# Optimization experiments

Measured on AMD Instinct MI355X. Metric: run time of the kernel, lower is better.

The kernel has to match this reference:

```python
import jax, jax.numpy as jnp
import numpy as np

B, L, T = 512, 1024, 128  # batch, seq_len, n_tags


def setup_inputs() -> dict:
    key = jax.random.key(0)
    k1, k2, k3 = jax.random.split(key, 3)
    return {
        "emit_scores": jax.random.normal(k1, (B, L, T), dtype=jnp.float32),
        "transitions": jax.random.normal(k2, (T, T), dtype=jnp.float32),
        "tag_weight": jax.random.uniform(k3, (T,), dtype=jnp.float32),
    }


def _viterbi_single(emit, transitions):
    # emit: [L, T] (already scaled by tag_weight); transitions: [T, T]
    def step(prev, obs):
        # scores[i, j] = prev[i] + obs[j] + transitions[i, j]
        scores = prev[:, None] + obs[None, :] + transitions  # [T, T]
        return jnp.max(scores, axis=0), jnp.argmax(scores, axis=0).astype(jnp.int32)

    prev, bps = jax.lax.scan(step, emit[0], emit[1:])  # bps: [L-1, T]
    best_score = jnp.max(prev)
    last = jnp.argmax(prev).astype(jnp.int32)

    # Backtrace: path[t] = bps[t][path[t+1]], path[L-1] = last
    def back(idx, bp):
        nidx = bp[idx]
        return nidx, nidx

    _, rev_path = jax.lax.scan(back, last, bps, reverse=True)  # [L-1]
    path = jnp.concatenate([rev_path, last[None]])  # [L]
    return path, best_score


def reference(emit_scores, transitions, tag_weight):
    # emit_scores *= tag_weight (broadcast over tag dim), matching the torch code
    emit = emit_scores * tag_weight  # [B, L, T]
    path, best_score = jax.vmap(_viterbi_single, in_axes=(0, None))(emit, transitions)
    # path: [B, L] int32 tag indices (the original maps these to tag strings);
    # best_score: [B] Viterbi max score.
    return path, best_score
```

## Files before the change

kernel.cpp:

```cpp
#include <hip/hip_runtime.h>

#define B 512
#define L 1024
#define T 128
#define NROWS (L - 1)
#define SEG 64
#define NSEG 16

typedef unsigned char u8;
typedef float f2 __attribute__((ext_vector_type(2)));

#if __has_builtin(__builtin_elementwise_max)
#define MAX2(a, b) __builtin_elementwise_max((a), (b))
#else
static __device__ __forceinline__ f2 max2_(f2 a, f2 b) {
    f2 r; r.x = fmaxf(a.x, b.x); r.y = fmaxf(a.y, b.y); return r;
}
#define MAX2(a, b) max2_((a), (b))
#endif
#define M3(a, b, c) fmaxf(fmaxf((a), (b)), (c))

#define BAR()                                                  \
    do {                                                       \
        asm volatile("s_waitcnt lgkmcnt(0)" ::: "memory");     \
        __builtin_amdgcn_s_barrier();                          \
        asm volatile("" ::: "memory");                         \
    } while (0)


__global__ __launch_bounds__(512, 4) void viterbi_fwd_val(
    const float* __restrict__ emit, const float* __restrict__ trans,
    const float* __restrict__ w, float* __restrict__ out,
    float* __restrict__ prevws, int* __restrict__ lastTag)
{
    const int b   = blockIdx.x;
    const int tid = threadIdx.x;
    const int h   = tid & 3;
    const int j   = tid >> 2;
    const int hbase = h << 5;
    const bool lane0 = (h == 0);

    __shared__ __align__(16) float prevbuf[2 * T];
    __shared__ float swv[8];
    __shared__ int   swj[8];

    f2 tc2[16];
#pragma unroll
    for (int q = 0; q < 8; ++q) {
        f2 a, c;
        a.x = trans[(size_t)(hbase + 4 * q + 0) * T + j];
        a.y = trans[(size_t)(hbase + 4 * q + 1) * T + j];
        c.x = trans[(size_t)(hbase + 4 * q + 2) * T + j];
        c.y = trans[(size_t)(hbase + 4 * q + 3) * T + j];
        tc2[2 * q] = a; tc2[2 * q + 1] = c;
    }

    const float wj = w[j];
    const size_t ebase = (size_t)b * L * T;
    float* prow = prevws + (size_t)b * NROWS * T;

    const char* prd = (const char*)prevbuf + 128 * h;
    char* pwr = (char*)prevbuf + 16 * ((j >> 2) ^ (j >> 5)) + 4 * (j & 3);

    const float e0 = emit[ebase + j] * wj;
    if (lane0) *(float*)pwr = e0;
    if (h == 1) prow[j] = e0;
    float myprev = e0;
    float r_c = emit[ebase + (size_t)T + j];
    float r_1 = emit[ebase + (size_t)2 * T + j];
    float bv_prev = 0.0f;
    BAR();

#define STEP(T_, ROFF_, WOFF_)                                                 \
    {                                                                          \
        const int t_ = (T_);                                                   \
        if (h == 1 && t_ >= 2)                                                 \
            prow[(size_t)(t_ - 1) * T + j] = bv_prev;                          \
        const int tn_ = (t_ + 2 < L) ? (t_ + 2) : (L - 1);                     \
        const float r_2 = emit[ebase + (size_t)tn_ * T + j];                   \
        const float obs_ = r_c * wj;                                           \
        f2 od_; od_.x = obs_; od_.y = obs_;                                    \
        f2 sv[16];                                                             \
        _Pragma("unroll")                                                      \
        for (int q = 0; q < 8; ++q) {                                          \
            const float4 p = *(const float4*)(prd + (ROFF_) + 16 * (q ^ h));   \
            f2 plo; plo.x = p.x; plo.y = p.y;                                  \
            f2 phi; phi.x = p.z; phi.y = p.w;                                  \
            sv[2 * q]     = (plo + od_) + tc2[2 * q];                          \
            sv[2 * q + 1] = (phi + od_) + tc2[2 * q + 1];                      \
        }                                                                      \
        const f2 a0 = MAX2(sv[0], sv[1]),   a1 = MAX2(sv[2], sv[3]);           \
        const f2 a2 = MAX2(sv[4], sv[5]),   a3 = MAX2(sv[6], sv[7]);           \
        const f2 a4 = MAX2(sv[8], sv[9]),   a5 = MAX2(sv[10], sv[11]);         \
        const f2 a6 = MAX2(sv[12], sv[13]), a7 = MAX2(sv[14], sv[15]);         \
        const f2 b0 = MAX2(a0, a1), b1 = MAX2(a2, a3);                         \
        const f2 b2 = MAX2(a4, a5), b3 = MAX2(a6, a7);                         \
        const f2 c0 = MAX2(b0, b1), c1 = MAX2(b2, b3);                         \
        const f2 d0 = MAX2(c0, c1);                                            \
        float bv = fmaxf(d0.x, d0.y);                                          \
        bv = fmaxf(bv, __shfl_xor(bv, 1));                                     \
        bv = fmaxf(bv, __shfl_xor(bv, 2));                                     \
        if (lane0) *(float*)(pwr + (WOFF_)) = bv;                              \
        myprev = bv;                                                           \
        bv_prev = bv;                                                          \
        r_c = r_1; r_1 = r_2;                                                  \
        BAR();                                                                 \
    }

    int t = 1;
    while (t + 1 < L) {
        STEP(t, 0, 512)
        STEP(t + 1, 512, 0)
        t += 2;
    }
    STEP(1023, 0, 512)
#undef STEP

    float rv = myprev; int rj = j;
#pragma unroll
    for (int m = 4; m <= 32; m <<= 1) {
        const float pv = __shfl_xor(rv, m);
        const int   pj = __shfl_xor(rj, m);
        if (pv > rv || (pv == rv && pj < rj)) { rv = pv; rj = pj; }
    }
    if ((tid & 63) == 0) { swv[tid >> 6] = rv; swj[tid >> 6] = rj; }
    __syncthreads();
    if (tid == 0) {
        float fv = swv[0]; int fj = swj[0];
#pragma unroll
        for (int wv = 1; wv < 8; ++wv) {
            if (swv[wv] > fv || (swv[wv] == fv && swj[wv] < fj)) {
                fv = swv[wv]; fj = swj[wv];
            }
        }
        out[(size_t)B * L + b] = fv;
        out[(size_t)b * L + (L - 1)] = (float)fj;
        lastTag[b] = fj;
    }
}

__global__ __launch_bounds__(64, 1) void backtrace(
    const float* __restrict__ emit, const float* __restrict__ trans,
    const float* __restrict__ w, const float* __restrict__ prevws,
    const int* __restrict__ lastTag, float* __restrict__ out)
{
    const int b = blockIdx.x;
    const int lane = threadIdx.x;
    __shared__ float transT[T * T];

#pragma unroll 4
    for (int it = 0; it < (T * T) / 64; ++it) {
        const int k = it * 64 + lane;
        const int i = k >> 7, jj = k & 127;
        transT[jj * T + (i ^ (jj & 31))] = trans[k];
    }

    const float w0 = w[lane], w1 = w[lane + 64];
    const size_t pbase = (size_t)b * NROWS * T;
    const size_t ebase = (size_t)b * L * T;
    const size_t obase = (size_t)b * L;

    float rp0[8], rp1[8], re0[8], re1[8];
#pragma unroll
    for (int k = 0; k < 8; ++k) {
        rp0[k] = prevws[pbase + (size_t)(1022 - k) * T + lane];
        rp1[k] = prevws[pbase + (size_t)(1022 - k) * T + lane + 64];
        re0[k] = emit[ebase + (size_t)(1023 - k) * T + lane];
        re1[k] = emit[ebase + (size_t)(1023 - k) * T + lane + 64];
    }

    int idx = lastTag[b];
    const float bsc = out[(size_t)B * L + b];
    float pp0 = bsc, pp1 = bsc;
    __syncthreads();

    int r = 1022;

#define BODY(U_)                                                               \
    {                                                                          \
        const float c0_ = rp0[U_], c1_ = rp1[U_];                              \
        const float e0_ = re0[U_], e1_ = re1[U_];                              \
        const int pr = (r >= 8) ? (r - 8) : 0;                                 \
        rp0[U_] = prevws[pbase + (size_t)pr * T + lane];                       \
        rp1[U_] = prevws[pbase + (size_t)pr * T + lane + 64];                  \
        re0[U_] = emit[ebase + (size_t)(pr + 1) * T + lane];                   \
        re1[U_] = emit[ebase + (size_t)(pr + 1) * T + lane + 64];              \
        const int sl = idx & 63;                                               \
        const bool lo = idx < 64;                                              \
        const float bv  = __shfl(lo ? pp0 : pp1, sl);                          \
        const float ew0 = e0_ * w0, ew1 = e1_ * w1;                            \
        const float obs = __shfl(lo ? ew0 : ew1, sl);                          \
        const int xc = lane ^ (idx & 31);                                      \
        const float t0 = transT[idx * T + xc];                                 \
        const float t1 = transT[idx * T + 64 + xc];                            \
        const float s0 = (c0_ + obs) + t0;                                     \
        const float s1 = (c1_ + obs) + t1;                                     \
        const unsigned long long m0 = __ballot(s0 == bv);                      \
        const unsigned long long m1 = __ballot(s1 == bv);                      \
        idx = (m0 != 0ULL) ? __builtin_ctzll(m0)                               \
                           : 64 + __builtin_ctzll(m1);                         \
        if (lane == 0) out[obase + r] = (float)idx;                            \
        pp0 = c0_; pp1 = c1_;                                                  \
        --r;                                                                   \
    }

#pragma unroll 1
    for (int g = 0; g < 127; ++g) {
        BODY(0) BODY(1) BODY(2) BODY(3) BODY(4) BODY(5) BODY(6) BODY(7)
    }
    BODY(0) BODY(1) BODY(2) BODY(3) BODY(4) BODY(5) BODY(6)
#undef BODY
}

__global__ __launch_bounds__(512, 4) void viterbi_fwd_slow(
    const float* __restrict__ emit, const float* __restrict__ trans,
    const float* __restrict__ w, float* __restrict__ out,
    u8* __restrict__ bps, int* __restrict__ lastTag)
{
    const int b   = blockIdx.x;
    const int tid = threadIdx.x;
    const int h   = tid & 3;
    const int j   = tid >> 2;
    const int hbase = h << 5;
    const bool lane0 = (h == 0);
    const int INF = 0x7fffffff;

    __shared__ __align__(16) float prevbuf[2 * T];
    __shared__ float swv[8];
    __shared__ int   swj[8];

    f2 tc2[16];
#pragma unroll
    for (int q = 0; q < 8; ++q) {
        f2 a, c;
        a.x = trans[(size_t)(hbase + 4 * q + 0) * T + j];
        a.y = trans[(size_t)(hbase + 4 * q + 1) * T + j];
        c.x = trans[(size_t)(hbase + 4 * q + 2) * T + j];
        c.y = trans[(size_t)(hbase + 4 * q + 3) * T + j];
        tc2[2 * q] = a; tc2[2 * q + 1] = c;
    }

    const float wj = w[j];
    const size_t ebase = (size_t)b * L * T;
    u8* bprow = bps + (size_t)b * NROWS * T;

    const char* prd = (const char*)prevbuf + 128 * h;
    char* pwr = (char*)prevbuf + 16 * ((j >> 2) ^ (j >> 5)) + 4 * (j & 3);

    const float e0 = emit[ebase + j] * wj;
    if (lane0) *(float*)pwr = e0;
    float myprev = e0;
    float raw_cur = emit[ebase + (size_t)T + j];
    int bidx_prev = 0;
    __syncthreads();

#define STEP(T_, ROFF_, WOFF_)                                                 \
    {                                                                          \
        const int t_ = (T_);                                                   \
        if (lane0 && t_ >= 2)                                                  \
            bprow[(size_t)(t_ - 2) * T + j] = (u8)bidx_prev;                   \
        const int tn_ = (t_ + 1 < L) ? (t_ + 1) : (L - 1);                     \
        const float raw_next_ = emit[ebase + (size_t)tn_ * T + j];             \
        const float obs_ = raw_cur * wj;                                       \
        f2 od_; od_.x = obs_; od_.y = obs_;                                    \
        f2 sv[16];                                                             \
        _Pragma("unroll")                                                      \
        for (int q = 0; q < 8; ++q) {                                          \
            const float4 p = *(const float4*)(prd + (ROFF_) + 16 * (q ^ h));   \
            f2 plo; plo.x = p.x; plo.y = p.y;                                  \
            f2 phi; phi.x = p.z; phi.y = p.w;                                  \
            sv[2 * q]     = (plo + od_) + tc2[2 * q];                          \
            sv[2 * q + 1] = (phi + od_) + tc2[2 * q + 1];                      \
        }                                                                      \
        float cm[4]; int loc[4];                                               \
        _Pragma("unroll")                                                      \
        for (int c = 0; c < 4; ++c) {                                          \
            const float s0 = sv[4 * c + 0].x, s1 = sv[4 * c + 0].y;            \
            const float s2 = sv[4 * c + 1].x, s3 = sv[4 * c + 1].y;            \
            const float s4 = sv[4 * c + 2].x, s5 = sv[4 * c + 2].y;            \
            const float s6 = sv[4 * c + 3].x, s7 = sv[4 * c + 3].y;            \
            const float m = M3(M3(s0, s1, s2), M3(s3, s4, s5),                 \
                               fmaxf(s6, s7));                                 \
            int k = 0;                                                         \
            k = (s7 == m) ? 7 : k; k = (s6 == m) ? 6 : k;                      \
            k = (s5 == m) ? 5 : k; k = (s4 == m) ? 4 : k;                      \
            k = (s3 == m) ? 3 : k; k = (s2 == m) ? 2 : k;                      \
            k = (s1 == m) ? 1 : k;                                             \
            cm[c] = m; loc[c] = 8 * c + k;                                     \
        }                                                                      \
        float bv = fmaxf(fmaxf(cm[0], cm[1]), fmaxf(cm[2], cm[3]));            \
        const int l0 = (cm[0] == bv) ? loc[0] : INF;                           \
        const int l1 = (cm[1] == bv) ? loc[1] : INF;                           \
        const int l2 = (cm[2] == bv) ? loc[2] : INF;                           \
        const int l3 = (cm[3] == bv) ? loc[3] : INF;                           \
        const int lm = min(min(min(l0, l1), l2), l3);                          \
        int gi = hbase + lm;                                                   \
        const float lv = bv;                                                   \
        bv = fmaxf(bv, __shfl_xor(bv, 1));                                     \
        bv = fmaxf(bv, __shfl_xor(bv, 2));                                     \
        int ii = (lv == bv) ? gi : INF;                                        \
        ii = min(ii, __shfl_xor(ii, 1));                                       \
        ii = min(ii, __shfl_xor(ii, 2));                                       \
        if (lane0) *(float*)(pwr + (WOFF_)) = bv;                              \
        myprev = bv;                                                           \
        bidx_prev = ii;                                                        \
        raw_cur = raw_next_;                                                   \
        __syncthreads();                                                       \
    }

    int t = 1;
    while (t + 1 < L) {
        STEP(t, 0, 512)
        STEP(t + 1, 512, 0)
        t += 2;
    }
    STEP(1023, 0, 512)
#undef STEP

    if (lane0) bprow[(size_t)(NROWS - 1) * T + j] = (u8)bidx_prev;

    float rv = myprev; int rj = j;
#pragma unroll
    for (int m = 4; m <= 32; m <<= 1) {
        const float pv = __shfl_xor(rv, m);
        const int   pj = __shfl_xor(rj, m);
        if (pv > rv || (pv == rv && pj < rj)) { rv = pv; rj = pj; }
    }
    if ((tid & 63) == 0) { swv[tid >> 6] = rv; swj[tid >> 6] = rj; }
    __syncthreads();
    if (tid == 0) {
        float fv = swv[0]; int fj = swj[0];
#pragma unroll
        for (int wv = 1; wv < 8; ++wv) {
            if (swv[wv] > fv || (swv[wv] == fv && swj[wv] < fj)) {
                fv = swv[wv]; fj = swj[wv];
            }
        }
        out[(size_t)B * L + b] = fv;
        out[(size_t)b * L + (L - 1)] = (float)fj;
        lastTag[b] = fj;
    }
}

__global__ __launch_bounds__(T) void segcomp(const u8* __restrict__ bps,
                                             u8* __restrict__ comp)
{
    const int s = blockIdx.x & (NSEG - 1);
    const int b = blockIdx.x >> 4;
    const int r0 = s * SEG;
    const int cnt = (NROWS - r0 < SEG) ? (NROWS - r0) : SEG;

    __shared__ __align__(16) u8 rows[SEG * T];
    const uint4* src = (const uint4*)(bps + ((size_t)b * NROWS + r0) * T);
    uint4* dst = (uint4*)rows;
    const int nvec = cnt * (T / 16);
    for (int k = threadIdx.x; k < nvec; k += T) dst[k] = src[k];
    __syncthreads();

    int x = threadIdx.x;
    for (int k = cnt - 1; k >= 0; --k) x = rows[k * T + x];
    comp[((size_t)b * NSEG + s) * T + threadIdx.x] = (u8)x;
}

__global__ void chainseg(const u8* __restrict__ comp,
                         const int* __restrict__ lastTag,
                         float* __restrict__ out)
{
    const int b = blockIdx.x * blockDim.x + threadIdx.x;
    if (b >= B) return;
    int e = lastTag[b];
#pragma unroll 1
    for (int s = NSEG - 1; s >= 0; --s) {
        e = comp[((size_t)b * NSEG + s) * T + e];
        out[(size_t)b * L + s * SEG] = (float)e;
    }
}

__global__ __launch_bounds__(T) void fillseg(const u8* __restrict__ bps,
                                             const int* __restrict__ lastTag,
                                             float* __restrict__ out)
{
    const int s = blockIdx.x & (NSEG - 1);
    const int b = blockIdx.x >> 4;
    const int r0 = s * SEG;
    const int cnt = (NROWS - r0 < SEG) ? (NROWS - r0) : SEG;

    __shared__ __align__(16) u8 rows[SEG * T];
    const uint4* src = (const uint4*)(bps + ((size_t)b * NROWS + r0) * T);
    uint4* dst = (uint4*)rows;
    const int nvec = cnt * (T / 16);
    for (int k = threadIdx.x; k < nvec; k += T) dst[k] = src[k];
    __syncthreads();

    if (threadIdx.x == 0) {
        int e = (s == NSEG - 1) ? lastTag[b]
                                : (int)out[(size_t)b * L + (size_t)(s + 1) * SEG];
        for (int k = cnt - 1; k >= 1; --k) {
            e = rows[k * T + e];
            out[(size_t)b * L + r0 + k] = (float)e;
        }
    }
}

extern "C" void kernel_launch(void* const* d_in, const int* in_sizes, int n_in,
                              void* d_out, int out_size, void* d_ws, size_t ws_size,
                              hipStream_t stream)
{
    const float* emit  = (const float*)d_in[0];
    const float* trans = (const float*)d_in[1];
    const float* w     = (const float*)d_in[2];
    float* out = (float*)d_out;

    const size_t prev_bytes = (size_t)B * NROWS * T * sizeof(float);
    const size_t need_fast  = prev_bytes + B * sizeof(int);

    if (ws_size >= need_fast) {
        float* prevws  = (float*)d_ws;
        int*   lastTag = (int*)((char*)d_ws + prev_bytes);
        viterbi_fwd_val<<<B, 512, 0, stream>>>(emit, trans, w, out, prevws, lastTag);
        backtrace<<<B, 64, 0, stream>>>(emit, trans, w, prevws, lastTag, out);
    } else {
        u8*  bps     = (u8*)d_ws;
        u8*  comp    = bps + (size_t)B * NROWS * T;
        int* lastTag = (int*)(comp + (size_t)B * NSEG * T);
        viterbi_fwd_slow<<<B, 512, 0, stream>>>(emit, trans, w, out, bps, lastTag);
        segcomp<<<B * NSEG, T, 0, stream>>>(bps, comp);
        chainseg<<<2, 256, 0, stream>>>(comp, lastTag, out);
        fillseg<<<B * NSEG, T, 0, stream>>>(bps, lastTag, out);
    }
}
```

Baseline: 877.7 us.

## Run forward Viterbi pass with one wavefront per sequence, dropping block barriers

The forward max-plus recursion now runs in a single 64-lane wavefront per batch element instead of a 512-thread block. Each lane owns two tags, keeps its full transition column in registers (256 floats), and uses packed adds and max3 inline asm. This removes per-step block barriers and the cross-lane shuffle reductions. In exchange each step does 32x more work per lane serially, register pressure is very high, and occupancy is limited to 512 waves total. The backtrace also gets a fallback when no lane matches.

```diff
diff --git a/kernel.cpp b/kernel.cpp
--- a/kernel.cpp
+++ b/kernel.cpp
@@ -10,15 +10,18 @@
 typedef unsigned char u8;
 typedef float f2 __attribute__((ext_vector_type(2)));
 
-#if __has_builtin(__builtin_elementwise_max)
-#define MAX2(a, b) __builtin_elementwise_max((a), (b))
-#else
-static __device__ __forceinline__ f2 max2_(f2 a, f2 b) {
-    f2 r; r.x = fmaxf(a.x, b.x); r.y = fmaxf(a.y, b.y); return r;
-}
-#define MAX2(a, b) max2_((a), (b))
-#endif
 #define M3(a, b, c) fmaxf(fmaxf((a), (b)), (c))
+
+static __device__ __forceinline__ f2 pkadd(f2 a, f2 b) {
+    f2 d;
+    asm("v_pk_add_f32 %0, %1, %2" : "=v"(d) : "v"(a), "v"(b));
+    return d;
+}
+static __device__ __forceinline__ float mx3(float a, float b, float c) {
+    float d;
+    asm("v_max3_f32 %0, %1, %2, %3" : "=v"(d) : "v"(a), "v"(b), "v"(c));
+    return d;
+}
 
 #define BAR()                                                  \
     do {                                                       \
@@ -27,115 +30,95 @@
         asm volatile("" ::: "memory");                         \
     } while (0)
 
-
-__global__ __launch_bounds__(512, 4) void viterbi_fwd_val(
+#define LDSFENCE() asm volatile("s_waitcnt lgkmcnt(0)" ::: "memory")
+
+
+__global__ __launch_bounds__(64, 1) void viterbi_fwd_val(
     const float* __restrict__ emit, const float* __restrict__ trans,
     const float* __restrict__ w, float* __restrict__ out,
     float* __restrict__ prevws, int* __restrict__ lastTag)
 {
-    const int b   = blockIdx.x;
-    const int tid = threadIdx.x;
-    const int h   = tid & 3;
-    const int j   = tid >> 2;
-    const int hbase = h << 5;
-    const bool lane0 = (h == 0);
-
-    __shared__ __align__(16) float prevbuf[2 * T];
-    __shared__ float swv[8];
-    __shared__ int   swj[8];
-
-    f2 tc2[16];
-#pragma unroll
-    for (int q = 0; q < 8; ++q) {
+    const int b = blockIdx.x;
+    const int j = threadIdx.x;
+
+    __shared__ __align__(16) float pb[T];
+
+    f2 trp0[64], trp1[64];
+#pragma unroll
+    for (int g = 0; g < 64; ++g) {
         f2 a, c;
-        a.x = trans[(size_t)(hbase + 4 * q + 0) * T + j];
-        a.y = trans[(size_t)(hbase + 4 * q + 1) * T + j];
-        c.x = trans[(size_t)(hbase + 4 * q + 2) * T + j];
-        c.y = trans[(size_t)(hbase + 4 * q + 3) * T + j];
-        tc2[2 * q] = a; tc2[2 * q + 1] = c;
-    }
-
-    const float wj = w[j];
-    const size_t ebase = (size_t)b * L * T;
+        a.x = trans[(size_t)(2 * g) * T + j];
+        a.y = trans[(size_t)(2 * g + 1) * T + j];
+        c.x = trans[(size_t)(2 * g) * T + j + 64];
+        c.y = trans[(size_t)(2 * g + 1) * T + j + 64];
+        trp0[g] = a; trp1[g] = c;
+    }
+
+    const float w0 = w[j], w1 = w[j + 64];
+    const size_t eb = (size_t)b * L * T;
     float* prow = prevws + (size_t)b * NROWS * T;
 
-    const char* prd = (const char*)prevbuf + 128 * h;
-    char* pwr = (char*)prevbuf + 16 * ((j >> 2) ^ (j >> 5)) + 4 * (j & 3);
-
-    const float e0 = emit[ebase + j] * wj;
-    if (lane0) *(float*)pwr = e0;
-    if (h == 1) prow[j] = e0;
-    float myprev = e0;
-    float r_c = emit[ebase + (size_t)T + j];
-    float r_1 = emit[ebase + (size_t)2 * T + j];
-    float bv_prev = 0.0f;
-    BAR();
-
-#define STEP(T_, ROFF_, WOFF_)                                                 \
+    float bv0 = emit[eb + j] * w0;
+    float bv1 = emit[eb + j + 64] * w1;
+    prow[j] = bv0; prow[j + 64] = bv1;
+
+    float rc0 = emit[eb + (size_t)T + j],     rc1 = emit[eb + (size_t)T + j + 64];
+    float r10 = emit[eb + (size_t)2 * T + j], r11 = emit[eb + (size_t)2 * T + j + 64];
+
+#define STEP_BODY(T_, STORE_)                                                  \
     {                                                                          \
         const int t_ = (T_);                                                   \
-        if (h == 1 && t_ >= 2)                                                 \
-            prow[(size_t)(t_ - 1) * T + j] = bv_prev;                          \
+        pb[j] = bv0; pb[j + 64] = bv1;                   \
         const int tn_ = (t_ + 2 < L) ? (t_ + 2) : (L - 1);                     \
-        const float r_2 = emit[ebase + (size_t)tn_ * T + j];                   \
-        const float obs_ = r_c * wj;                                           \
-        f2 od_; od_.x = obs_; od_.y = obs_;                                    \
-        f2 sv[16];                                                             \
+        const float r20 = emit[eb + (size_t)tn_ * T + j];                      \
+        const float r21 = emit[eb + (size_t)tn_ * T + j + 64];                 \
+        const float obs0 = rc0 * w0, obs1 = rc1 * w1;                          \
+        f2 od0; od0.x = obs0; od0.y = obs0;                                    \
+        f2 od1; od1.x = obs1; od1.y = obs1;                                    \
+        float a0 = -3.4e38f, a1 = -3.4e38f, a2 = -3.4e38f, a3 = -3.4e38f;      \
+        LDSFENCE();                                   \
         _Pragma("unroll")                                                      \
-        for (int q = 0; q < 8; ++q) {                                          \
-            const float4 p = *(const float4*)(prd + (ROFF_) + 16 * (q ^ h));   \
+        for (int g = 0; g < 32; ++g) {                                         \
+            const float4 p = *(const float4*)&pb[4 * g];        \
             f2 plo; plo.x = p.x; plo.y = p.y;                                  \
             f2 phi; phi.x = p.z; phi.y = p.w;                                  \
-            sv[2 * q]     = (plo + od_) + tc2[2 * q];                          \
-            sv[2 * q + 1] = (phi + od_) + tc2[2 * q + 1];                      \
+            const f2 sA0 = pkadd(pkadd(plo, od0), trp0[2 * g]);                \
+            const f2 sA1 = pkadd(pkadd(phi, od0), trp0[2 * g + 1]);            \
+            const f2 sB0 = pkadd(pkadd(plo, od1), trp1[2 * g]);                \
+            const f2 sB1 = pkadd(pkadd(phi, od1), trp1[2 * g + 1]);            \
+            a0 = mx3(a0, sA0.x, sA0.y);                                        \
+            a1 = mx3(a1, sA1.x, sA1.y);                                        \
+            a2 = mx3(a2, sB0.x, sB0.y);                                        \
+            a3 = mx3(a3, sB1.x, sB1.y);                                        \
         }                                                                      \
-        const f2 a0 = MAX2(sv[0], sv[1]),   a1 = MAX2(sv[2], sv[3]);           \
-        const f2 a2 = MAX2(sv[4], sv[5]),   a3 = MAX2(sv[6], sv[7]);           \
-        const f2 a4 = MAX2(sv[8], sv[9]),   a5 = MAX2(sv[10], sv[11]);         \
-        const f2 a6 = MAX2(sv[12], sv[13]), a7 = MAX2(sv[14], sv[15]);         \
-        const f2 b0 = MAX2(a0, a1), b1 = MAX2(a2, a3);                         \
-        const f2 b2 = MAX2(a4, a5), b3 = MAX2(a6, a7);                         \
-        const f2 c0 = MAX2(b0, b1), c1 = MAX2(b2, b3);                         \
-        const f2 d0 = MAX2(c0, c1);                                            \
-        float bv = fmaxf(d0.x, d0.y);                                          \
-        bv = fmaxf(bv, __shfl_xor(bv, 1));                                     \
-        bv = fmaxf(bv, __shfl_xor(bv, 2));                                     \
-        if (lane0) *(float*)(pwr + (WOFF_)) = bv;                              \
-        myprev = bv;                                                           \
-        bv_prev = bv;                                                          \
-        r_c = r_1; r_1 = r_2;                                                  \
-        BAR();                                                                 \
-    }
-
-    int t = 1;
-    while (t + 1 < L) {
-        STEP(t, 0, 512)
-        STEP(t + 1, 512, 0)
-        t += 2;
-    }
-    STEP(1023, 0, 512)
-#undef STEP
-
-    float rv = myprev; int rj = j;
-#pragma unroll
-    for (int m = 4; m <= 32; m <<= 1) {
+        const float nb0 = fmaxf(a0, a1);                                       \
+        const float nb1 = fmaxf(a2, a3);                                       \
+        if (STORE_) {                                                          \
+            prow[(size_t)t_ * T + j] = nb0;                                    \
+            prow[(size_t)t_ * T + j + 64] = nb1;                               \
+        }                                                                      \
+        bv0 = nb0; bv1 = nb1;                                                  \
+        rc0 = r10; r10 = r20;                                                  \
+        rc1 = r11; r11 = r21;                                                  \
+    }
+
+#pragma unroll 1
+    for (int t = 1; t < L - 1; ++t) STEP_BODY(t, true)
+    STEP_BODY(L - 1, false)
+#undef STEP_BODY
+
+    float rv; int rj;
+    if (bv1 > bv0) { rv = bv1; rj = j + 64; } else { rv = bv0; rj = j; }
+#pragma unroll
+    for (int m = 1; m <= 32; m <<= 1) {
         const float pv = __shfl_xor(rv, m);
         const int   pj = __shfl_xor(rj, m);
         if (pv > rv || (pv == rv && pj < rj)) { rv = pv; rj = pj; }
     }
-    if ((tid & 63) == 0) { swv[tid >> 6] = rv; swj[tid >> 6] = rj; }
-    __syncthreads();
-    if (tid == 0) {
-        float fv = swv[0]; int fj = swj[0];
-#pragma unroll
-        for (int wv = 1; wv < 8; ++wv) {
-            if (swv[wv] > fv || (swv[wv] == fv && swj[wv] < fj)) {
-                fv = swv[wv]; fj = swj[wv];
-            }
-        }
-        out[(size_t)B * L + b] = fv;
-        out[(size_t)b * L + (L - 1)] = (float)fj;
-        lastTag[b] = fj;
+    if (j == 0) {
+        out[(size_t)B * L + b] = rv;
+        out[(size_t)b * L + (L - 1)] = (float)rj;
+        lastTag[b] = rj;
     }
 }
 
@@ -198,7 +181,7 @@
         const unsigned long long m0 = __ballot(s0 == bv);                      \
         const unsigned long long m1 = __ballot(s1 == bv);                      \
         idx = (m0 != 0ULL) ? __builtin_ctzll(m0)                               \
-                           : 64 + __builtin_ctzll(m1);                         \
+            : ((m1 != 0ULL) ? 64 + __builtin_ctzll(m1) : idx);                 \
         if (lane == 0) out[obase + r] = (float)idx;                            \
         pp0 = c0_; pp1 = c1_;                                                  \
         --r;                                                                   \
@@ -417,7 +400,7 @@
     if (ws_size >= need_fast) {
         float* prevws  = (float*)d_ws;
         int*   lastTag = (int*)((char*)d_ws + prev_bytes);
-        viterbi_fwd_val<<<B, 512, 0, stream>>>(emit, trans, w, out, prevws, lastTag);
+        viterbi_fwd_val<<<B, 64, 0, stream>>>(emit, trans, w, out, prevws, lastTag);
         backtrace<<<B, 64, 0, stream>>>(emit, trans, w, prevws, lastTag, out);
     } else {
         u8*  bps     = (u8*)d_ws;
```

New measurement: 2.125 ms. 142% more time.
